# Performance work log

Hardware: AMD Instinct MI355X
Metric: run time of the kernel (lower is better)

## Reference

```python
import jax, jax.numpy as jnp
import numpy as np

NT_SIZES = {"paper": 100000, "author": 200000, "subject": 1000}
NT_FEATS = {"paper": 512, "author": 256, "subject": 128}
ET = [("paper", "author"), ("author", "paper"), ("paper", "subject"), ("subject", "paper")]
E_COUNTS = {("paper", "author"): 800000, ("author", "paper"): 800000,
            ("paper", "subject"): 100000, ("subject", "paper"): 100000}
HOP = 5
NHID = 64
NOUT = 16
# edge types sourced at each node type (order follows ET / edge_id mapping)
SRC_IDS = {"paper": [0, 2], "author": [1], "subject": [3]}


def setup_inputs() -> dict:
    key = jax.random.key(0)
    ks = iter(jax.random.split(key, 40))
    inp = {}
    # node features
    inp["x_paper"] = jax.random.normal(next(ks), (NT_SIZES["paper"], NT_FEATS["paper"]), jnp.float32)
    inp["x_author"] = jax.random.normal(next(ks), (NT_SIZES["author"], NT_FEATS["author"]), jnp.float32)
    inp["x_subject"] = jax.random.normal(next(ks), (NT_SIZES["subject"], NT_FEATS["subject"]), jnp.float32)
    # fc1 per node type (torch Linear layout: [out, in]), scaled ~1/sqrt(fan_in)
    for nt in NT_SIZES:
        fin = NT_FEATS[nt]
        inp[f"fc1_{nt}_w"] = jax.random.normal(next(ks), (NHID, fin), jnp.float32) / np.sqrt(fin)
        inp[f"fc1_{nt}_b"] = jnp.zeros((NHID,), jnp.float32)
    # attention vectors per hop per edge type; small scale keeps exp() stable
    inp["attn1_w"] = jax.random.normal(next(ks), (HOP, len(ET), NHID), jnp.float32) * 0.01
    inp["attn2_w"] = jax.random.normal(next(ks), (HOP, len(ET), NHID), jnp.float32) * 0.01
    inp["lw_w"] = jax.random.normal(next(ks), (HOP, len(ET)), jnp.float32)
    inp["fc2_w"] = jax.random.normal(next(ks), (NOUT, NHID), jnp.float32) / np.sqrt(NHID)
    inp["fc2_b"] = jnp.zeros((NOUT,), jnp.float32)
    # edge indices: row 0 = source (in src node-type range), row 1 = target
    for (s_nt, t_nt) in ET:
        E = E_COUNTS[(s_nt, t_nt)]
        s = jax.random.randint(next(ks), (E,), 0, NT_SIZES[s_nt], jnp.int32)
        t = jax.random.randint(next(ks), (E,), 0, NT_SIZES[t_nt], jnp.int32)
        inp[f"ei_{s_nt[0]}{t_nt[0]}"] = jnp.stack([s, t])
    return inp


def reference(x_paper, x_author, x_subject,
              fc1_paper_w, fc1_paper_b, fc1_author_w, fc1_author_b,
              fc1_subject_w, fc1_subject_b,
              attn1_w, attn2_w, lw_w, fc2_w, fc2_b,
              ei_pa, ei_ap, ei_ps, ei_sp):
    x_in = {"paper": x_paper, "author": x_author, "subject": x_subject}
    fc1 = {"paper": (fc1_paper_w, fc1_paper_b),
           "author": (fc1_author_w, fc1_author_b),
           "subject": (fc1_subject_w, fc1_subject_b)}
    edges = {ET[0]: ei_pa, ET[1]: ei_ap, ET[2]: ei_ps, ET[3]: ei_sp}

    # input projection (dropout = identity in eval mode)
    x_dict = {nt: jax.nn.relu(x_in[nt] @ fc1[nt][0].T + fc1[nt][1]) for nt in x_in}
    h_dict = dict(x_dict)

    for i in range(HOP):
        aggr = {nt: [] for nt in x_dict}
        for k, et in enumerate(ET):
            s_nt, t_nt = et
            ei = edges[et]
            s, t = ei[0], ei[1]
            x = x_dict[s_nt]            # [Ns, D]
            h = h_dict[t_nt]            # [Nt, D]
            N = x.shape[0]
            a1 = attn1_w[i, k]          # [D]
            a2 = attn2_w[i, k]          # [D]
            x1 = x @ a1                 # [Ns]
            h1 = h @ a2                 # [Nt]
            w2 = jnp.exp(jax.nn.leaky_relu(x1 + x @ a2, 0.2))            # [Ns] self term
            w1 = jnp.exp(jax.nn.leaky_relu(x1[s] + h1[t], 0.2))          # [E]  edge term
            div = jax.ops.segment_sum(w1, s, num_segments=N) + w2        # [Ns]
            num = jax.ops.segment_sum(w1[:, None] * h[t], s, num_segments=N) + w2[:, None] * x
            aggr[s_nt].append(num / div[:, None])
        for nt in x_dict:
            ids = jnp.array(SRC_IDS[nt])
            w = jax.nn.softmax(lw_w[i, ids])                             # learnable per-edge-type mix
            stacked = jnp.stack(aggr[nt], axis=1)                        # [N, K, D]
            h_dict[nt] = jax.nn.elu(jnp.einsum('nkd,k->nd', stacked, w))
    return h_dict["paper"] @ fc2_w.T + fc2_b
```

## Files before the change

kernel.cpp:

```cpp
#include <hip/hip_runtime.h>
#include <hip/hip_bf16.h>


#define NP 100000
#define NA 200000
#define NSJ 1000
#define EPA 800000
#define EAP 800000
#define EPS 100000
#define ESP 100000
#define ETOT 1800000
#define NS_TOT 401000
#define NSRC 301000
#define NCHUNK 392
#define NSGRP 25063
#define SCAT_SLICE 4096
#define NSLICE ((ETOT + SCAT_SLICE - 1) / SCAT_SLICE)
#define BKT ((ETOT + 7) / 8)

typedef __attribute__((ext_vector_type(8))) short bf16x8;
typedef __attribute__((ext_vector_type(4))) float floatx4;
typedef __attribute__((ext_vector_type(8))) float floatx8;
typedef __hip_bfloat16 bf16;

__device__ __forceinline__ float bf2f(bf16 v) { return __bfloat162float(v); }
__device__ __forceinline__ float us2f(unsigned short u) { return __uint_as_float((unsigned)u << 16); }
__device__ __forceinline__ float eluf(float x) { return x > 0.f ? x : __expf(x) - 1.f; }
__device__ __forceinline__ unsigned short f2bf_bits(float f) {
    unsigned int u = __float_as_uint(f);
    return (unsigned short)((u + 0x7FFFu + ((u >> 16) & 1u)) >> 16);
}

__device__ __forceinline__ void gload_lds16(const void* g, void* l) {
    __builtin_amdgcn_global_load_lds(
        (const __attribute__((address_space(1))) unsigned int*)g,
        (__attribute__((address_space(3))) unsigned int*)l, 16, 0, 0);
}

__device__ __forceinline__ bf16x8 load_frag_f32(const void* base, size_t off) {
    const float4* f = (const float4*)((const float*)base + off);
    float4 a = f[0], b = f[1];
    bf16x8 r;
    r[0] = (short)f2bf_bits(a.x); r[1] = (short)f2bf_bits(a.y);
    r[2] = (short)f2bf_bits(a.z); r[3] = (short)f2bf_bits(a.w);
    r[4] = (short)f2bf_bits(b.x); r[5] = (short)f2bf_bits(b.y);
    r[6] = (short)f2bf_bits(b.z); r[7] = (short)f2bf_bits(b.w);
    return r;
}

__device__ __forceinline__ int edge_src(int e, const int* pa, const int* ap,
                                        const int* ps, const int* sp) {
    if (e < EPA)                  return pa[e];
    if (e < EPA + EAP)            return NP + ap[e - EPA];
    if (e < EPA + EAP + EPS)      return NP + NA + ps[e - (EPA + EAP)];
    return NP + NA + NP + sp[e - (EPA + EAP + EPS)];
}
__device__ __forceinline__ int edge_tgt(int e, const int* pa, const int* ap,
                                        const int* ps, const int* sp) {
    if (e < EPA)                  return pa[EPA + e];
    if (e < EPA + EAP)            return ap[EAP + (e - EPA)];
    if (e < EPA + EAP + EPS)      return ps[EPS + (e - (EPA + EAP))];
    return sp[ESP + (e - (EPA + EAP + EPS))];
}

__global__ void detect_dtype(const unsigned int* __restrict__ xraw, int* __restrict__ flag) {
    int t = threadIdx.x;
    int hits = 0;
#pragma unroll
    for (int i = 0; i < 16; ++i) {
        unsigned int w = xraw[t * 16 + i];
        unsigned int lo = w & 0xFFFFu;
        unsigned int e = (lo >> 7) & 0xFFu;
        if (lo == 0u || (e >= 110u && e <= 140u)) hits++;
    }
#pragma unroll
    for (int o = 32; o; o >>= 1) hits += __shfl_xor(hits, o);
    if (t == 0) *flag = (hits > 512) ? 1 : 0;
}

__global__ void conv_all(const void* a1, const void* a2, const void* lw, const void* w2,
                         const void* b2, const void* bp, const void* ba, const void* bs,
                         float* a1c, float* a2c, float* lwc, float* w2c, float* b2c,
                         float* b1p, float* b1a, float* b1s, const int* __restrict__ flagp)
{
    int i = blockIdx.x * blockDim.x + threadIdx.x;
    int isb = *flagp;
    auto cv = [&](const void* s, int j) -> float {
        return isb ? bf2f(((const bf16*)s)[j]) : ((const float*)s)[j];
    };
    if (i < 1280)      a1c[i] = cv(a1, i);
    else if (i < 2560) a2c[i - 1280] = cv(a2, i - 1280);
    else if (i < 2580) lwc[i - 2560] = cv(lw, i - 2560);
    else if (i < 3604) w2c[i - 2580] = cv(w2, i - 2580);
    else if (i < 3620) b2c[i - 3604] = cv(b2, i - 3604);
    else if (i < 3684) b1p[i - 3620] = cv(bp, i - 3620);
    else if (i < 3748) b1a[i - 3684] = cv(ba, i - 3684);
    else if (i < 3812) b1s[i - 3748] = cv(bs, i - 3748);
}

__global__ void pack_attn(const float* __restrict__ a1c, const float* __restrict__ a2c,
                          bf16* __restrict__ apack)
{
    int i = blockIdx.x * blockDim.x + threadIdx.x;
    if (i >= 4096) return;
    int k = i >> 10, rf = i & 1023;
    int row = rf >> 6;
    int f = rf & 63;
    float v = 0.f;
    if (row < 5)       v = a1c[(row * 4 + k) * 64 + f];
    else if (row < 10) v = a2c[((row - 5) * 4 + k) * 64 + f];
    unsigned short hi = f2bf_bits(v);
    float lo = v - us2f(hi);
    unsigned short* up = (unsigned short*)apack;
    up[(size_t)(k * 2) * 1024 + rf]     = hi;
    up[(size_t)(k * 2 + 1) * 1024 + rf] = f2bf_bits(lo);
}

template<int K>
__global__ void fc1_lds(const void* __restrict__ X, const void* __restrict__ W,
                        const float* __restrict__ Bb, int N,
                        bf16* __restrict__ xo, const int* __restrict__ flagp)
{
    constexpr int NSTEP = K / 128;
    __shared__ __align__(16) unsigned char lds[2][64 * 256];
    int isb = *flagp;
    int lane = threadIdx.x & 63;
    int wv = threadIdx.x >> 6;
    int row0 = blockIdx.x * 64;
    int m = lane & 15, kq = lane >> 4;
    floatx4 acc[4] = {};

    if (isb) {
        const bf16* Xb = (const bf16*)X;
        const bf16* Wb = (const bf16*)W;
        auto stage = [&](int s, int b) {
#pragma unroll
            for (int it = 0; it < 4; ++it) {
                int slotbase = (it * 4 + wv) * 64;
                int slot = slotbase + lane;
                int r = slot >> 4;
                int c = slot & 15;
                int rc = row0 + r; if (rc >= N) rc = N - 1;
                int cs = c ^ (r & 15);
                const bf16* src = Xb + (size_t)rc * K + s * 128 + cs * 8;
                gload_lds16(src, &lds[b][slotbase * 16]);
            }
        };
        stage(0, 0);
        asm volatile("s_waitcnt vmcnt(0)" ::: "memory");
        __syncthreads();
        int R = wv * 16 + m;
#pragma unroll
        for (int s = 0; s < NSTEP; ++s) {
            if (s + 1 < NSTEP) stage(s + 1, (s + 1) & 1);
            const unsigned char* bufp = lds[s & 1];
#pragma unroll
            for (int i = 0; i < 4; ++i) {
                int cs = (i * 4 + kq) ^ (R & 15);
                bf16x8 av = *(const bf16x8*)(bufp + R * 256 + cs * 16);
                int kg = s * 128 + i * 32 + kq * 8;
#pragma unroll
                for (int nb = 0; nb < 4; ++nb) {
                    bf16x8 bv = *(const bf16x8*)(Wb + (size_t)(nb * 16 + m) * K + kg);
                    acc[nb] = __builtin_amdgcn_mfma_f32_16x16x32_bf16(av, bv, acc[nb], 0, 0, 0);
                }
            }
            asm volatile("s_waitcnt vmcnt(0)" ::: "memory");
            __syncthreads();
        }
    } else {
        int arow = row0 + wv * 16 + m;
        if (arow >= N) arow = N - 1;
#pragma unroll 4
        for (int i = 0; i < K / 32; ++i) {
            int k0 = i * 32 + kq * 8;
            bf16x8 av = load_frag_f32(X, (size_t)arow * K + k0);
#pragma unroll
            for (int nb = 0; nb < 4; ++nb) {
                bf16x8 bv = load_frag_f32(W, (size_t)(nb * 16 + m) * K + k0);
                acc[nb] = __builtin_amdgcn_mfma_f32_16x16x32_bf16(av, bv, acc[nb], 0, 0, 0);
            }
        }
    }
#pragma unroll
    for (int nb = 0; nb < 4; ++nb) {
#pragma unroll
        for (int r = 0; r < 4; ++r) {
            int row = row0 + wv * 16 + kq * 4 + r;
            if (row < N) {
                int f = nb * 16 + m;
                float v = acc[nb][r] + Bb[f];
                xo[(size_t)row * 64 + f] = __float2bfloat16(fmaxf(v, 0.f));
            }
        }
    }
}

__global__ void precompute_xw_mfma(const bf16* __restrict__ xP, const bf16* __restrict__ xA,
                                   const bf16* __restrict__ xS,
                                   const bf16* __restrict__ apack,
                                   float* __restrict__ x1buf, float* __restrict__ w2buf)
{
    int wv = threadIdx.x >> 6;
    int lane = threadIdx.x & 63;
    int grp = blockIdx.x * 4 + wv;
    if (grp >= NSGRP) return;
    int base = grp * 16;
    int k, n0, nmax; const bf16* x;
    if (base < NP)                { k = 0; n0 = base;                  nmax = NP;  x = xP; }
    else if (base < NP + NA)      { k = 1; n0 = base - NP;             nmax = NA;  x = xA; }
    else if (base < NP + NA + NP) { k = 2; n0 = base - (NP + NA);      nmax = NP;  x = xP; }
    else                          { k = 3; n0 = base - (NP + NA + NP); nmax = NSJ; x = xS; }
    int m = lane & 15, kq = lane >> 4;
    int arow = n0 + m;
    if (arow >= nmax) arow = nmax - 1;
    const bf16* bh = apack + (size_t)(k * 2) * 1024;
    const bf16* bl = bh + 1024;
    floatx4 acc = {};
#pragma unroll
    for (int ks = 0; ks < 64; ks += 32) {
        int k0 = ks + kq * 8;
        bf16x8 av  = *(const bf16x8*)(x  + (size_t)arow * 64 + k0);
        bf16x8 bvh = *(const bf16x8*)(bh + m * 64 + k0);
        bf16x8 bvl = *(const bf16x8*)(bl + m * 64 + k0);
        acc = __builtin_amdgcn_mfma_f32_16x16x32_bf16(av, bvh, acc, 0, 0, 0);
        acc = __builtin_amdgcn_mfma_f32_16x16x32_bf16(av, bvl, acc, 0, 0, 0);
    }
#pragma unroll
    for (int r = 0; r < 4; ++r) {
        float v = acc[r];
        float d2 = __shfl(v, lane + 5);
        int node = base + kq * 4 + r;
        if (m < 5 && node < NS_TOT) {
            x1buf[m * NS_TOT + node] = v;
            float z = v + d2;
            w2buf[m * NS_TOT + node] = __expf(z > 0.f ? z : 0.2f * z);
        }
    }
}

__global__ void csr_rank(const int* __restrict__ pa, const int* __restrict__ ap,
                         const int* __restrict__ ps, const int* __restrict__ sp,
                         int* __restrict__ cnt, int* __restrict__ rank)
{
    int e = blockIdx.x * blockDim.x + threadIdx.x;
    if (e >= ETOT) return;
    int g = edge_src(e, pa, ap, ps, sp);
    rank[e] = atomicAdd(&cnt[g], 1);
}

__global__ void scan_reduce(const int* __restrict__ cnt, int* __restrict__ partial)
{
    __shared__ int s[256];
    int base = blockIdx.x * 1024 + threadIdx.x * 4;
    int sum = 0;
#pragma unroll
    for (int r = 0; r < 4; ++r) { int i = base + r; if (i < NS_TOT) sum += cnt[i]; }
    s[threadIdx.x] = sum; __syncthreads();
    for (int o = 128; o; o >>= 1) {
        if (threadIdx.x < o) s[threadIdx.x] += s[threadIdx.x + o];
        __syncthreads();
    }
    if (!threadIdx.x) partial[blockIdx.x] = s[0];
}

__global__ void scan_partials(const int* __restrict__ partial, int* __restrict__ chunkoff)
{
    __shared__ int s[512];
    int t = threadIdx.x;
    int v = (t < NCHUNK) ? partial[t] : 0;
    s[t] = v; __syncthreads();
    for (int o = 1; o < 512; o <<= 1) {
        int add = (t >= o) ? s[t - o] : 0;
        __syncthreads();
        s[t] += add; __syncthreads();
    }
    if (t < NCHUNK) chunkoff[t] = s[t] - v;
}

__global__ void scan_write(const int* __restrict__ cnt, const int* __restrict__ chunkoff,
                           int* __restrict__ off)
{
    __shared__ int s[256];
    int t = threadIdx.x;
    int base = blockIdx.x * 1024 + t * 4;
    int v[4]; int tsum = 0;
#pragma unroll
    for (int r = 0; r < 4; ++r) { int i = base + r; v[r] = (i < NS_TOT) ? cnt[i] : 0; tsum += v[r]; }
    s[t] = tsum; __syncthreads();
    for (int o = 1; o < 256; o <<= 1) {
        int add = (t >= o) ? s[t - o] : 0;
        __syncthreads();
        s[t] += add; __syncthreads();
    }
    int excl = s[t] - tsum + chunkoff[blockIdx.x];
#pragma unroll
    for (int r = 0; r < 4; ++r) {
        int i = base + r;
        if (i < NS_TOT) { off[i] = excl; excl += v[r]; }
    }
}

__global__ void csr_pos(const int* __restrict__ pa, const int* __restrict__ ap,
                        const int* __restrict__ ps, const int* __restrict__ sp,
                        const int* __restrict__ rank, const int* __restrict__ off,
                        int* __restrict__ pos)
{
    int e = blockIdx.x * blockDim.x + threadIdx.x;
    if (e >= ETOT) return;
    int g = edge_src(e, pa, ap, ps, sp);
    pos[e] = off[g] + rank[e];
}

__global__ void csr_scatter(const int* __restrict__ pa, const int* __restrict__ ap,
                            const int* __restrict__ ps, const int* __restrict__ sp,
                            const int* __restrict__ pos, int* __restrict__ col)
{
    int b = blockIdx.x & 7;
    int slice = blockIdx.x >> 3;
    int lo = b * BKT;
    int hi = lo + BKT; if (hi > ETOT) hi = ETOT;
    int ebase = slice * SCAT_SLICE;
    int eend = ebase + SCAT_SLICE; if (eend > ETOT) eend = ETOT;
    for (int e = ebase + threadIdx.x; e < eend; e += 256) {
        int p = pos[e];
        if (p < lo || p >= hi) continue;
        col[p] = edge_tgt(e, pa, ap, ps, sp);
    }
}

__device__ __forceinline__ floatx8 agg_et8(int g, int hop, int k, int eo, int fl, floatx8 xv,
    const float* __restrict__ x1buf, const float* __restrict__ w2buf,
    const float* __restrict__ a2c, const bf16* __restrict__ ht,
    const int* __restrict__ off, const int* __restrict__ deg, const int* __restrict__ col)
{
    float x1v = x1buf[hop * NS_TOT + g];
    const float4* a2p = (const float4*)(a2c + (hop * 4 + k) * 64 + fl * 8);
    float4 a2a = a2p[0], a2b = a2p[1];
    floatx8 acc = {};
    float dv = 0.f;
    int e0 = off[g];
    int e1 = e0 + deg[g];
    for (int e = e0 + eo; e < e1; e += 8) {
        int t = col[e];
        bf16x8 hv = *(const bf16x8*)(ht + (size_t)t * 64 + fl * 8);
        float hf[8];
#pragma unroll
        for (int j = 0; j < 8; ++j) hf[j] = us2f((unsigned short)hv[j]);
        float h1t = hf[0] * a2a.x;
        h1t = fmaf(hf[1], a2a.y, h1t); h1t = fmaf(hf[2], a2a.z, h1t);
        h1t = fmaf(hf[3], a2a.w, h1t); h1t = fmaf(hf[4], a2b.x, h1t);
        h1t = fmaf(hf[5], a2b.y, h1t); h1t = fmaf(hf[6], a2b.z, h1t);
        h1t = fmaf(hf[7], a2b.w, h1t);
        h1t += __shfl_xor(h1t, 1);
        h1t += __shfl_xor(h1t, 2);
        h1t += __shfl_xor(h1t, 4);
        float z = x1v + h1t;
        float w1 = __expf(z > 0.f ? z : 0.2f * z);
#pragma unroll
        for (int j = 0; j < 8; ++j) acc[j] = fmaf(w1, hf[j], acc[j]);
        dv += w1;
    }
#pragma unroll
    for (int o = 8; o <= 32; o <<= 1) {
#pragma unroll
        for (int j = 0; j < 8; ++j) acc[j] += __shfl_xor(acc[j], o);
        dv += __shfl_xor(dv, o);
    }
    float w2v = w2buf[hop * NS_TOT + g];
    dv += w2v;
    float inv = 1.f / dv;
    floatx8 r;
#pragma unroll
    for (int j = 0; j < 8; ++j) r[j] = (acc[j] + w2v * xv[j]) * inv;
    return r;
}

__global__ void hop_agg(const bf16* __restrict__ hPo, const bf16* __restrict__ hAo,
                        const bf16* __restrict__ hSo,
                        const bf16* __restrict__ xP, const bf16* __restrict__ xA,
                        const bf16* __restrict__ xS,
                        const float* __restrict__ x1buf, const float* __restrict__ w2buf,
                        const float* __restrict__ a2c,
                        const int* __restrict__ off, const int* __restrict__ deg,
                        const int* __restrict__ col,
                        const float* __restrict__ lw, int hop,
                        bf16* __restrict__ hPn, bf16* __restrict__ hAn, bf16* __restrict__ hSn)
{
    int wid = (blockIdx.x * blockDim.x + threadIdx.x) >> 6;
    int lane = threadIdx.x & 63;
    int eo = lane >> 3, fl = lane & 7;
    if (wid >= NSRC) return;
    floatx8 r;
    bf16* dst;
    int n;
    if (wid < NP) {
        n = wid;
        bf16x8 xu = *(const bf16x8*)(xP + (size_t)n * 64 + fl * 8);
        floatx8 xv;
#pragma unroll
        for (int j = 0; j < 8; ++j) xv[j] = us2f((unsigned short)xu[j]);
        floatx8 r0 = agg_et8(n,           hop, 0, eo, fl, xv, x1buf, w2buf, a2c, hAo, off, deg, col);
        floatx8 r2 = agg_et8(NP + NA + n, hop, 2, eo, fl, xv, x1buf, w2buf, a2c, hSo, off, deg, col);
        float l0 = lw[hop * 4 + 0], l2 = lw[hop * 4 + 2];
        float mx = fmaxf(l0, l2);
        float e0 = __expf(l0 - mx), e2 = __expf(l2 - mx);
        float inv = 1.f / (e0 + e2);
#pragma unroll
        for (int j = 0; j < 8; ++j) r[j] = (e0 * r0[j] + e2 * r2[j]) * inv;
        dst = hPn;
    } else if (wid < NP + NA) {
        n = wid - NP;
        bf16x8 xu = *(const bf16x8*)(xA + (size_t)n * 64 + fl * 8);
        floatx8 xv;
#pragma unroll
        for (int j = 0; j < 8; ++j) xv[j] = us2f((unsigned short)xu[j]);
        r = agg_et8(NP + n, hop, 1, eo, fl, xv, x1buf, w2buf, a2c, hPo, off, deg, col);
        dst = hAn;
    } else {
        n = wid - (NP + NA);
        bf16x8 xu = *(const bf16x8*)(xS + (size_t)n * 64 + fl * 8);
        floatx8 xv;
#pragma unroll
        for (int j = 0; j < 8; ++j) xv[j] = us2f((unsigned short)xu[j]);
        r = agg_et8(NP + NA + NP + n, hop, 3, eo, fl, xv, x1buf, w2buf, a2c, hPo, off, deg, col);
        dst = hSn;
    }
    if (eo == 0) {
        bf16x8 st;
#pragma unroll
        for (int j = 0; j < 8; ++j) st[j] = (short)f2bf_bits(eluf(r[j]));
        *(bf16x8*)(dst + (size_t)n * 64 + fl * 8) = st;
    }
}

__global__ void fc2_kernel(const bf16* __restrict__ hP, const float* __restrict__ W2,
                           const float* __restrict__ B2, void* __restrict__ out,
                           const int* __restrict__ flagp)
{
    int isb = *flagp;
    int idx = blockIdx.x * blockDim.x + threadIdx.x;
    if (idx >= NP * 16) return;
    int n = idx >> 4, o = idx & 15;
    float acc = B2[o];
    const bf16* hr = hP + (size_t)n * 64;
#pragma unroll
    for (int j = 0; j < 64; ++j) acc = fmaf(bf2f(hr[j]), W2[o * 64 + j], acc);
    if (isb) ((bf16*)out)[idx] = __float2bfloat16(acc);
    else     ((float*)out)[idx] = acc;
}

extern "C" void kernel_launch(void* const* d_in, const int* in_sizes, int n_in,
                              void* d_out, int out_size, void* d_ws, size_t ws_size,
                              hipStream_t stream)
{
    (void)in_sizes; (void)n_in; (void)out_size; (void)ws_size;
    const void* xPi  = d_in[0];
    const void* xAi  = d_in[1];
    const void* xSi  = d_in[2];
    const void* f1pw = d_in[3];
    const void* f1pb = d_in[4];
    const void* f1aw = d_in[5];
    const void* f1ab = d_in[6];
    const void* f1sw = d_in[7];
    const void* f1sb = d_in[8];
    const void* attn1 = d_in[9];
    const void* attn2 = d_in[10];
    const void* lwp  = d_in[11];
    const void* f2w  = d_in[12];
    const void* f2b  = d_in[13];
    const int* eipa = (const int*)d_in[14];
    const int* eiap = (const int*)d_in[15];
    const int* eips = (const int*)d_in[16];
    const int* eisp = (const int*)d_in[17];

    char* p = (char*)d_ws;
    auto alloc = [&](size_t bytes) { char* r = p; p += (bytes + 255) & ~(size_t)255; return r; };
    int*  flag = (int*)alloc(4);
    bf16* xP = (bf16*)alloc((size_t)NP * 64 * 2);
    bf16* xA = (bf16*)alloc((size_t)NA * 64 * 2);
    bf16* xS = (bf16*)alloc((size_t)NSJ * 64 * 2);
    bf16* hb[2][3];
    for (int qq = 0; qq < 2; ++qq) {
        hb[qq][0] = (bf16*)alloc((size_t)NP * 64 * 2);
        hb[qq][1] = (bf16*)alloc((size_t)NA * 64 * 2);
        hb[qq][2] = (bf16*)alloc((size_t)NSJ * 64 * 2);
    }
    float* x1buf = (float*)alloc((size_t)5 * NS_TOT * 4);
    float* w2buf = (float*)alloc((size_t)5 * NS_TOT * 4);
    int* cnt   = (int*)alloc((size_t)NS_TOT * 4);
    int* off   = (int*)alloc((size_t)NS_TOT * 4);
    int* rankv = (int*)alloc((size_t)ETOT * 4);
    int* posv  = (int*)alloc((size_t)ETOT * 4);
    int* colv  = (int*)alloc((size_t)ETOT * 4);
    int* partial  = (int*)alloc(512 * 4);
    int* chunkoff = (int*)alloc(512 * 4);
    float* a1c = (float*)alloc(1280 * 4);
    float* a2c = (float*)alloc(1280 * 4);
    float* lwc = (float*)alloc(20 * 4);
    float* w2c = (float*)alloc(1024 * 4);
    float* b2c = (float*)alloc(16 * 4);
    float* b1p = (float*)alloc(64 * 4);
    float* b1a = (float*)alloc(64 * 4);
    float* b1s = (float*)alloc(64 * 4);
    bf16* apack = (bf16*)alloc((size_t)4 * 2 * 1024 * 2);

    detect_dtype<<<1, 64, 0, stream>>>((const unsigned int*)xPi, flag);
    conv_all<<<15, 256, 0, stream>>>(attn1, attn2, lwp, f2w, f2b, f1pb, f1ab, f1sb,
                                     a1c, a2c, lwc, w2c, b2c, b1p, b1a, b1s, flag);
    pack_attn<<<16, 256, 0, stream>>>(a1c, a2c, apack);

    fc1_lds<512><<<(NP + 63) / 64, 256, 0, stream>>>(xPi, f1pw, b1p, NP, xP, flag);
    fc1_lds<256><<<(NA + 63) / 64, 256, 0, stream>>>(xAi, f1aw, b1a, NA, xA, flag);
    fc1_lds<128><<<(NSJ + 63) / 64, 256, 0, stream>>>(xSi, f1sw, b1s, NSJ, xS, flag);

    precompute_xw_mfma<<<(NSGRP + 3) / 4, 256, 0, stream>>>(xP, xA, xS, apack, x1buf, w2buf);

    hipMemsetAsync(cnt, 0, (size_t)NS_TOT * 4, stream);
    csr_rank<<<(ETOT + 255) / 256, 256, 0, stream>>>(eipa, eiap, eips, eisp, cnt, rankv);
    scan_reduce<<<NCHUNK, 256, 0, stream>>>(cnt, partial);
    scan_partials<<<1, 512, 0, stream>>>(partial, chunkoff);
    scan_write<<<NCHUNK, 256, 0, stream>>>(cnt, chunkoff, off);
    csr_pos<<<(ETOT + 255) / 256, 256, 0, stream>>>(eipa, eiap, eips, eisp, rankv, off, posv);
    csr_scatter<<<NSLICE * 8, 256, 0, stream>>>(eipa, eiap, eips, eisp, posv, colv);

    const bf16* cP = xP; const bf16* cA = xA; const bf16* cS = xS;
    for (int i = 0; i < 5; ++i) {
        bf16* nPb = hb[i & 1][0]; bf16* nAb = hb[i & 1][1]; bf16* nSb = hb[i & 1][2];
        hop_agg<<<(NSRC + 3) / 4, 256, 0, stream>>>(cP, cA, cS, xP, xA, xS,
                                                    x1buf, w2buf, a2c, off, cnt, colv,
                                                    lwc, i, nPb, nAb, nSb);
        cP = nPb; cA = nAb; cS = nSb;
    }

    fc2_kernel<<<(NP * 16 + 255) / 256, 256, 0, stream>>>(cP, w2c, b2c, d_out, flag);
}
```

Baseline: 1.657 ms.

## Precompute per-target attention scores per hop and pack four nodes per wave

Adds a per-hop kernel that computes h·a2 once for every target node of each edge type, instead of recomputing that dot product for every edge inside the aggregation. The aggregation kernel then reads one scalar per edge for the attention weight. It also changes the layout from one source node per 64-lane wave with 8 edge lanes to four nodes per wave with 2 edge lanes each, which cuts shuffle reductions and idle lanes for low-degree nodes. The cost is an extra launch and a small buffer per hop, and less edge parallelism for high-degree nodes.

```diff
diff --git a/kernel.cpp b/kernel.cpp
--- a/kernel.cpp
+++ b/kernel.cpp
@@ -11,6 +11,7 @@
 #define ESP 100000
 #define ETOT 1800000
 #define NS_TOT 401000
+#define NT_TOT 401000
 #define NSRC 301000
 #define NCHUNK 392
 #define NSGRP 25063
@@ -329,44 +330,61 @@
     }
 }
 
-__device__ __forceinline__ floatx8 agg_et8(int g, int hop, int k, int eo, int fl, floatx8 xv,
+__global__ void hop_h1(const bf16* __restrict__ hP, const bf16* __restrict__ hA,
+                       const bf16* __restrict__ hS,
+                       const float* __restrict__ a2c, int hop, float* __restrict__ h1)
+{
+    int wave = (blockIdx.x * blockDim.x + threadIdx.x) >> 6;
+    int lane = threadIdx.x & 63;
+    int eo = lane >> 3, fl = lane & 7;
+    int wid = wave * 8 + eo;
+    if (wid >= NT_TOT) return;
+    int k, n; const bf16* h;
+    if (wid < NA)                 { k = 0; n = wid;               h = hA; }
+    else if (wid < NA + NP)       { k = 1; n = wid - NA;          h = hP; }
+    else if (wid < NA + NP + NSJ) { k = 2; n = wid - (NA + NP);   h = hS; }
+    else                          { k = 3; n = wid - (NA+NP+NSJ); h = hP; }
+    bf16x8 hv = *(const bf16x8*)(h + (size_t)n * 64 + fl * 8);
+    const float4* a2p = (const float4*)(a2c + (hop * 4 + k) * 64 + fl * 8);
+    float4 aa = a2p[0], ab = a2p[1];
+    float v = us2f((unsigned short)hv[0]) * aa.x;
+    v = fmaf(us2f((unsigned short)hv[1]), aa.y, v);
+    v = fmaf(us2f((unsigned short)hv[2]), aa.z, v);
+    v = fmaf(us2f((unsigned short)hv[3]), aa.w, v);
+    v = fmaf(us2f((unsigned short)hv[4]), ab.x, v);
+    v = fmaf(us2f((unsigned short)hv[5]), ab.y, v);
+    v = fmaf(us2f((unsigned short)hv[6]), ab.z, v);
+    v = fmaf(us2f((unsigned short)hv[7]), ab.w, v);
+    v += __shfl_xor(v, 1);
+    v += __shfl_xor(v, 2);
+    v += __shfl_xor(v, 4);
+    if (fl == 0) h1[wid] = v;
+}
+
+__device__ __forceinline__ floatx8 agg_et16(int g, int hop, int eo2, int fl, floatx8 xv,
     const float* __restrict__ x1buf, const float* __restrict__ w2buf,
-    const float* __restrict__ a2c, const bf16* __restrict__ ht,
+    const float* __restrict__ h1, int h1base, const bf16* __restrict__ ht,
     const int* __restrict__ off, const int* __restrict__ deg, const int* __restrict__ col)
 {
     float x1v = x1buf[hop * NS_TOT + g];
-    const float4* a2p = (const float4*)(a2c + (hop * 4 + k) * 64 + fl * 8);
-    float4 a2a = a2p[0], a2b = a2p[1];
+    const float* h1p = h1 + h1base;
     floatx8 acc = {};
     float dv = 0.f;
     int e0 = off[g];
     int e1 = e0 + deg[g];
-    for (int e = e0 + eo; e < e1; e += 8) {
+    for (int e = e0 + eo2; e < e1; e += 2) {
         int t = col[e];
+        float z = x1v + h1p[t];
+        float w1 = __expf(z > 0.f ? z : 0.2f * z);
         bf16x8 hv = *(const bf16x8*)(ht + (size_t)t * 64 + fl * 8);
-        float hf[8];
-#pragma unroll
-        for (int j = 0; j < 8; ++j) hf[j] = us2f((unsigned short)hv[j]);
-        float h1t = hf[0] * a2a.x;
-        h1t = fmaf(hf[1], a2a.y, h1t); h1t = fmaf(hf[2], a2a.z, h1t);
-        h1t = fmaf(hf[3], a2a.w, h1t); h1t = fmaf(hf[4], a2b.x, h1t);
-        h1t = fmaf(hf[5], a2b.y, h1t); h1t = fmaf(hf[6], a2b.z, h1t);
-        h1t = fmaf(hf[7], a2b.w, h1t);
-        h1t += __shfl_xor(h1t, 1);
-        h1t += __shfl_xor(h1t, 2);
-        h1t += __shfl_xor(h1t, 4);
-        float z = x1v + h1t;
-        float w1 = __expf(z > 0.f ? z : 0.2f * z);
-#pragma unroll
-        for (int j = 0; j < 8; ++j) acc[j] = fmaf(w1, hf[j], acc[j]);
+#pragma unroll
+        for (int j = 0; j < 8; ++j)
+            acc[j] = fmaf(w1, us2f((unsigned short)hv[j]), acc[j]);
         dv += w1;
     }
 #pragma unroll
-    for (int o = 8; o <= 32; o <<= 1) {
-#pragma unroll
-        for (int j = 0; j < 8; ++j) acc[j] += __shfl_xor(acc[j], o);
-        dv += __shfl_xor(dv, o);
-    }
+    for (int j = 0; j < 8; ++j) acc[j] += __shfl_xor(acc[j], 8);
+    dv += __shfl_xor(dv, 8);
     float w2v = w2buf[hop * NS_TOT + g];
     dv += w2v;
     float inv = 1.f / dv;
@@ -381,15 +399,18 @@
                         const bf16* __restrict__ xP, const bf16* __restrict__ xA,
                         const bf16* __restrict__ xS,
                         const float* __restrict__ x1buf, const float* __restrict__ w2buf,
-                        const float* __restrict__ a2c,
+                        const float* __restrict__ h1,
                         const int* __restrict__ off, const int* __restrict__ deg,
                         const int* __restrict__ col,
                         const float* __restrict__ lw, int hop,
                         bf16* __restrict__ hPn, bf16* __restrict__ hAn, bf16* __restrict__ hSn)
 {
-    int wid = (blockIdx.x * blockDim.x + threadIdx.x) >> 6;
+    int wave = (blockIdx.x * blockDim.x + threadIdx.x) >> 6;
     int lane = threadIdx.x & 63;
-    int eo = lane >> 3, fl = lane & 7;
+    int seg = lane >> 4;
+    int l16 = lane & 15;
+    int eo2 = l16 >> 3, fl = l16 & 7;
+    int wid = wave * 4 + seg;
     if (wid >= NSRC) return;
     floatx8 r;
     bf16* dst;
@@ -400,8 +421,8 @@
         floatx8 xv;
 #pragma unroll
         for (int j = 0; j < 8; ++j) xv[j] = us2f((unsigned short)xu[j]);
-        floatx8 r0 = agg_et8(n,           hop, 0, eo, fl, xv, x1buf, w2buf, a2c, hAo, off, deg, col);
-        floatx8 r2 = agg_et8(NP + NA + n, hop, 2, eo, fl, xv, x1buf, w2buf, a2c, hSo, off, deg, col);
+        floatx8 r0 = agg_et16(n,           hop, eo2, fl, xv, x1buf, w2buf, h1, 0,       hAo, off, deg, col);
+        floatx8 r2 = agg_et16(NP + NA + n, hop, eo2, fl, xv, x1buf, w2buf, h1, NA + NP, hSo, off, deg, col);
         float l0 = lw[hop * 4 + 0], l2 = lw[hop * 4 + 2];
         float mx = fmaxf(l0, l2);
         float e0 = __expf(l0 - mx), e2 = __expf(l2 - mx);
@@ -415,7 +436,7 @@
         floatx8 xv;
 #pragma unroll
         for (int j = 0; j < 8; ++j) xv[j] = us2f((unsigned short)xu[j]);
-        r = agg_et8(NP + n, hop, 1, eo, fl, xv, x1buf, w2buf, a2c, hPo, off, deg, col);
+        r = agg_et16(NP + n, hop, eo2, fl, xv, x1buf, w2buf, h1, NA, hPo, off, deg, col);
         dst = hAn;
     } else {
         n = wid - (NP + NA);
@@ -423,10 +444,10 @@
         floatx8 xv;
 #pragma unroll
         for (int j = 0; j < 8; ++j) xv[j] = us2f((unsigned short)xu[j]);
-        r = agg_et8(NP + NA + NP + n, hop, 3, eo, fl, xv, x1buf, w2buf, a2c, hPo, off, deg, col);
+        r = agg_et16(NP + NA + NP + n, hop, eo2, fl, xv, x1buf, w2buf, h1, NA + NP + NSJ, hPo, off, deg, col);
         dst = hSn;
     }
-    if (eo == 0) {
+    if (eo2 == 0) {
         bf16x8 st;
 #pragma unroll
         for (int j = 0; j < 8; ++j) st[j] = (short)f2bf_bits(eluf(r[j]));
@@ -488,6 +509,7 @@
     }
     float* x1buf = (float*)alloc((size_t)5 * NS_TOT * 4);
     float* w2buf = (float*)alloc((size_t)5 * NS_TOT * 4);
+    float* h1v  = (float*)alloc((size_t)NT_TOT * 4);
     int* cnt   = (int*)alloc((size_t)NS_TOT * 4);
     int* off   = (int*)alloc((size_t)NS_TOT * 4);
     int* rankv = (int*)alloc((size_t)ETOT * 4);
@@ -527,8 +549,9 @@
     const bf16* cP = xP; const bf16* cA = xA; const bf16* cS = xS;
     for (int i = 0; i < 5; ++i) {
         bf16* nPb = hb[i & 1][0]; bf16* nAb = hb[i & 1][1]; bf16* nSb = hb[i & 1][2];
-        hop_agg<<<(NSRC + 3) / 4, 256, 0, stream>>>(cP, cA, cS, xP, xA, xS,
-                                                    x1buf, w2buf, a2c, off, cnt, colv,
+        hop_h1<<<(NT_TOT / 8 + 4) / 4, 256, 0, stream>>>(cP, cA, cS, a2c, i, h1v);
+        hop_agg<<<((NSRC + 3) / 4 + 3) / 4, 256, 0, stream>>>(cP, cA, cS, xP, xA, xS,
+                                                    x1buf, w2buf, h1v, off, cnt, colv,
                                                     lwc, i, nPb, nAb, nSb);
         cP = nPb; cA = nAb; cS = nSb;
     }
```

Measured after the change: 1.382 ms. -16.6%, faster.
